# Performance work log

Hardware: AMD Instinct MI355X
Metric: run time of the kernel (lower is better)

Reference implementation:

```python
import jax, jax.numpy as jnp
import numpy as np
import math

B, T, C, H, LC, DFF = 2, 1024, 1024, 16, 256, 4096
EPS = 1e-6


def _ln(x):
    # LayerNorm without affine (elementwise_affine=False under AdaLN), eps=1e-6
    m = jnp.mean(x, -1, keepdims=True)
    v = jnp.mean((x - m) ** 2, -1, keepdims=True)
    return (x - m) * jax.lax.rsqrt(v + EPS)


def _heads(t):
    b, l, c = t.shape
    return t.reshape(b, l, H, c // H).transpose(0, 2, 1, 3)  # (b,H,l,dh)


def _unheads(t):
    b, h, l, d = t.shape
    return t.transpose(0, 2, 1, 3).reshape(b, l, h * d)


def setup_inputs():
    key = jax.random.key(0)
    ks = jax.random.split(key, 16)
    s = 0.02
    p = lambda k, sh: jax.random.normal(k, sh, jnp.float32) * s
    x_star = jax.random.normal(ks[0], (B, T, C), jnp.float32)
    x_hat = jax.random.normal(ks[1], (B, T, C), jnp.float32)
    c = jax.random.normal(ks[2], (B, LC, C), jnp.float32)
    chunk = jnp.sort(jax.random.randint(ks[3], (B, T), 0, 32), axis=1)
    m_star = chunk[:, :, None] > chunk[:, None, :]   # attend to strictly earlier chunks
    m_hat = chunk[:, :, None] == chunk[:, None, :]   # attend within same chunk
    dep_mask = jax.random.bernoulli(ks[4], 0.98, (B, T, T)) | jnp.eye(T, dtype=bool)[None]
    return dict(
        x_star=x_star, x_hat=x_hat, c=c,
        m_star=m_star, m_hat=m_hat, dep_mask=dep_mask,
        ncond_g=jnp.ones((C,), jnp.float32), ncond_b=jnp.zeros((C,), jnp.float32),
        Wq=p(ks[5], (C, C)), bq=jnp.zeros((C,), jnp.float32),
        Wkv=p(ks[6], (C, 2 * C)), bkv=jnp.zeros((2 * C,), jnp.float32),
        Wco=p(ks[7], (C, C)), bco=jnp.zeros((C,), jnp.float32),
        Wada=p(ks[8], (C, 6 * C)), bada=jnp.zeros((6 * C,), jnp.float32),
        Wqkv=p(ks[9], (C, 3 * C)), bqkv=jnp.zeros((3 * C,), jnp.float32),
        Wo=p(ks[10], (C, C)), bo=jnp.zeros((C,), jnp.float32),
        W1=p(ks[11], (C, DFF)), b1=jnp.zeros((DFF,), jnp.float32),
        W2=p(ks[12], (DFF, C)), b2=jnp.zeros((C,), jnp.float32),
    )


def _cross_attn(x, c, Wq, bq, Wkv, bkv, Wco, bco):
    q = _heads(x @ Wq + bq)
    k, v = jnp.split(c @ Wkv + bkv, 2, -1)
    k, v = _heads(k), _heads(v)
    att = jnp.einsum('bhtd,bhsd->bhts', q, k) / math.sqrt(C // H)
    y = jnp.einsum('bhts,bhsd->bhtd', jax.nn.softmax(att, -1), v)
    return _unheads(y) @ Wco + bco


def _interleave(xs, xh, m_star, m_hat, dep, Wqkv, bqkv, Wo, bo):
    # Attention.forward_interleave (eval: dropout identity)
    NEG = -jnp.inf
    sc = 1.0 / math.sqrt(C // H)
    qkv = lambda x: [_heads(t) for t in jnp.split(x @ Wqkv + bqkv, 3, -1)]
    qs, ks, vs = qkv(xs)
    qh, kh, vh = qkv(xh)
    blk_star = (~m_star)[:, None]     # True -> block
    blk_hat = (~m_hat)[:, None]
    blk_dep = (~dep)[:, None]
    causal = jnp.triu(jnp.ones((T, T), bool), 1)[None, None]
    # star stream: causal + dependency mask
    att_star = jnp.einsum('bhtd,bhsd->bhts', qs, ks) * sc
    att_star = jnp.where(blk_dep, NEG, att_star)
    p_star = jax.nn.softmax(jnp.where(causal, NEG, att_star), -1)
    y_star = _unheads(jnp.einsum('bhts,bhsd->bhtd', p_star, vs)) @ Wo + bo
    # hat stream: merge logits (q_hat vs k_star on earlier chunks, q_hat vs k_hat within chunk)
    a1 = jnp.where(blk_star, NEG, jnp.einsum('bhtd,bhsd->bhts', qh, ks) * sc)
    a2 = jnp.where(blk_hat, NEG, jnp.einsum('bhtd,bhsd->bhts', qh, kh) * sc)
    merged = jnp.where(jnp.isinf(a2), a1, a2)
    merged = jnp.where(blk_dep, NEG, merged)
    p_hat = jax.nn.softmax(merged, -1)
    y_hat = jnp.einsum('bhts,bhsd->bhtd', jnp.where(blk_star, 0.0, p_hat), vs) \
          + jnp.einsum('bhts,bhsd->bhtd', jnp.where(blk_hat, 0.0, p_hat), vh)
    y_hat = _unheads(y_hat) @ Wo + bo
    return y_star, y_hat


def reference(x_star, x_hat, c, m_star, m_hat, dep_mask,
              ncond_g, ncond_b, Wq, bq, Wkv, bkv, Wco, bco, Wada, bada,
              Wqkv, bqkv, Wo, bo, W1, b1, W2, b2):
    mod = lambda x, sh, scale: x * (1 + scale) + sh
    mlp = lambda x: jax.nn.gelu(x @ W1 + b1, approximate=True) @ W2 + b2
    ca = lambda x: _cross_attn(_ln(x) * ncond_g + ncond_b, c, Wq, bq, Wkv, bkv, Wco, bco)
    ada = lambda t: jnp.split(jax.nn.silu(t) @ Wada + bada, 6, -1)
    gs = ada(ca(x_star))
    gh = ada(ca(x_hat))
    ms = mod(_ln(x_star), gs[0], gs[1])
    mh = mod(_ln(x_hat), gh[0], gh[1])
    ys, yh = _interleave(ms, mh, m_star, m_hat, dep_mask, Wqkv, bqkv, Wo, bo)
    x_star = x_star + gs[2] * ys
    x_hat = x_hat + gh[2] * yh
    x_star = x_star + gs[5] * mlp(mod(_ln(x_star), gs[3], gs[4]))
    x_hat = x_hat + gh[5] * mlp(mod(_ln(x_hat), gh[3], gh[4]))
    return x_star, x_hat
```

## Files before the change

kernel.cpp:

```cpp
#include <hip/hip_runtime.h>
#include <hip/hip_bf16.h>
#include <stdint.h>

#define DEVI __device__ __forceinline__

typedef __bf16 bf16x8 __attribute__((ext_vector_type(8)));
typedef float f32x4 __attribute__((ext_vector_type(4)));
typedef unsigned short us;
typedef unsigned long long ull;

DEVI float b2f(us u) { union { unsigned int i; float f; } v; v.i = ((unsigned int)u) << 16; return v.f; }
DEVI us f2b(float f) {
  union { unsigned int i; float f; } v; v.f = f;
  unsigned int r = (v.i + 0x7fffu + ((v.i >> 16) & 1u)) >> 16;
  return (us)r;
}

#define NEGINF (-__builtin_inff())

DEVI void gl2lds16(const us* g, us* l) {
  __builtin_amdgcn_global_load_lds(
      (const __attribute__((address_space(1))) unsigned int*)g,
      (__attribute__((address_space(3))) unsigned int*)l, 16, 0, 0);
}

__global__ __launch_bounds__(256) void detect_flags(
    const unsigned int* __restrict__ xw, const unsigned int* __restrict__ mw,
    int* __restrict__ flags) {
  const int t = threadIdx.x;
  int cnt = 0, big = 0;
  for (int i = t; i < 4096; i += 256) {
    unsigned int w = xw[i];
    us lo = (us)(w & 0xffffu);
    float a = fabsf(b2f(lo));
    cnt += ((lo == 0) || (a >= 1e-8f && a <= 256.f)) ? 1 : 0;
    big |= (mw[i] > 1u) ? 1 : 0;
  }
  for (int o = 32; o; o >>= 1) { cnt += __shfl_down(cnt, o); big |= __shfl_down(big, o); }
  __shared__ int sc[4], sb[4];
  if ((t & 63) == 0) { sc[t >> 6] = cnt; sb[t >> 6] = big; }
  __syncthreads();
  if (t == 0) {
    flags[0] = (sc[0] + sc[1] + sc[2] + sc[3] < 2048) ? 1 : 0;
    flags[1] = (sb[0] | sb[1] | sb[2] | sb[3]);
  }
}

__global__ __launch_bounds__(256) void cvt_bf16(
    const void* __restrict__ src, us* __restrict__ dst, int n,
    const int* __restrict__ flags) {
  const int f32mode = flags[0];
  int idx = (blockIdx.x * 256 + threadIdx.x) * 4;
  if (idx >= n) return;
  if (f32mode) {
    const float* s = (const float*)src;
    float4 v = *(const float4*)(s + idx);
    dst[idx] = f2b(v.x); dst[idx + 1] = f2b(v.y);
    dst[idx + 2] = f2b(v.z); dst[idx + 3] = f2b(v.w);
  } else {
    *(uint2*)(dst + idx) = *(const uint2*)((const us*)src + idx);
  }
}

struct P10 { const void* p[10]; };
__global__ __launch_bounds__(256) void cvt_small(P10 ps, us* __restrict__ dst,
                                                 const int* __restrict__ flags) {
  const int offs[11] = {0, 1024, 2048, 3072, 5120, 6144, 12288, 15360, 16384, 20480, 21504};
  int idx = blockIdx.x * 256 + threadIdx.x;
  if (idx >= 21504) return;
  int seg = 0;
#pragma unroll
  for (int i = 1; i < 10; ++i) seg += (idx >= offs[i]) ? 1 : 0;
  int local = idx - offs[seg];
  float v = flags[0] ? ((const float*)ps.p[seg])[local]
                     : b2f(((const us*)ps.p[seg])[local]);
  dst[idx] = f2b(v);
}

__global__ __launch_bounds__(256) void transpose_cvt64(
    const void* __restrict__ W, us* __restrict__ WT, int K, int N,
    const int* __restrict__ flags) {
  __shared__ __attribute__((aligned(16))) us tile[64 * 72];
  const int f32m = flags[0];
  const int k0 = blockIdx.x * 64, n0 = blockIdx.y * 64;
  const int t = threadIdx.x;
  const int row = t >> 2, colb = (t & 3) * 16;
  const int sw = ((row >> 4) & 3) << 4;
  us tmp[16];
  if (f32m) {
    const float* src = (const float*)W + (size_t)(k0 + row) * N + n0 + colb;
#pragma unroll
    for (int i = 0; i < 16; i += 4) {
      float4 v = *(const float4*)(src + i);
      tmp[i] = f2b(v.x); tmp[i + 1] = f2b(v.y); tmp[i + 2] = f2b(v.z); tmp[i + 3] = f2b(v.w);
    }
  } else {
    const us* src = (const us*)W + (size_t)(k0 + row) * N + n0 + colb;
    *(uint4*)tmp = *(const uint4*)src;
    *(uint4*)(tmp + 8) = *(const uint4*)(src + 8);
  }
  *(uint4*)&tile[row * 72 + (colb ^ sw)] = *(uint4*)tmp;
  *(uint4*)&tile[row * 72 + (colb ^ sw) + 8] = *(uint4*)(tmp + 8);
  __syncthreads();
  const int orow = t >> 2, ocolb = (t & 3) * 16;
  const int pc = (orow & 15) | ((orow & 48) ^ (ocolb & 48));
  us out[16];
#pragma unroll
  for (int i = 0; i < 16; ++i) out[i] = tile[(ocolb + i) * 72 + pc];
  us* dst = WT + (size_t)(n0 + orow) * K + k0 + ocolb;
  *(uint4*)dst = *(uint4*)out;
  *(uint4*)(dst + 8) = *(uint4*)(out + 8);
}

struct P3 { const void* p[3]; };
__global__ __launch_bounds__(256) void pack_mask3(P3 ms, ull* __restrict__ bits,
                                                  const int* __restrict__ flags) {
  const int bytemode = flags[1];
  const void* m = ms.p[blockIdx.y];
  ull* out = bits + (size_t)blockIdx.y * 32768;
  int wv = blockIdx.x * 4 + (threadIdx.x >> 6);
  int lane = threadIdx.x & 63;
  for (int w = 0; w < 16; ++w) {
    int v;
    if (bytemode) v = ((const unsigned char*)m)[(size_t)wv * 1024 + w * 64 + lane];
    else          v = ((const int*)m)[(size_t)wv * 1024 + w * 64 + lane];
    ull b = __ballot(v != 0);
    if (lane == 0) out[(size_t)wv * 16 + w] = b;
  }
}

__global__ __launch_bounds__(256) void hat_blockflags(
    const ull* __restrict__ starb, const ull* __restrict__ hatb, int* __restrict__ bf) {
  const int bt = blockIdx.x;
  const int b = bt >> 4, tt = bt & 15;
  const int t = threadIdx.x, wv = t >> 6, lane = t & 63;
  const int t0 = tt * 64;
  for (int k = 0; k < 4; ++k) {
    int ck = wv * 4 + k;
    ull sw = starb[(size_t)(b * 1024 + t0 + lane) * 16 + ck];
    ull hw = hatb[(size_t)(b * 1024 + t0 + lane) * 16 + ck];
    int f = (__ballot(sw != 0ull) ? 1 : 0) | (__ballot(hw != 0ull) ? 2 : 0);
    if (lane == 0) bf[bt * 16 + ck] = f;
  }
}

__global__ __launch_bounds__(256) void vtrans(
    const us* __restrict__ src, us* __restrict__ dst,
    int T, int stride, int colBase, int rowOff) {
  __shared__ __attribute__((aligned(16))) us tile[64][65];
  const int bh = blockIdx.y, b = bh >> 4, h = bh & 15;
  const int t0 = blockIdx.x * 64;
  const int t = threadIdx.x;
#pragma unroll
  for (int it = 0; it < 2; ++it) {
    int idx = it * 256 + t; int r = idx >> 3, c8 = (idx & 7) * 8;
    uint4 d4 = *(const uint4*)(src + (size_t)(rowOff + b * T + t0 + r) * stride + colBase + h * 64 + c8);
    const us* e = (const us*)&d4;
#pragma unroll
    for (int i = 0; i < 8; ++i) tile[r][c8 + i] = e[i];
  }
  __syncthreads();
#pragma unroll
  for (int it = 0; it < 2; ++it) {
    int idx = it * 256 + t; int d = idx >> 3, c8 = (idx & 7) * 8;
    us tmp[8];
#pragma unroll
    for (int i = 0; i < 8; ++i) tmp[i] = tile[c8 + i][d];
    *(uint4*)(dst + ((size_t)(bh * 64 + d)) * T + t0 + c8) = *(const uint4*)tmp;
  }
}

__global__ __launch_bounds__(256) void ln_affine(
    const void* __restrict__ xs, const void* __restrict__ xh,
    const us* __restrict__ gw, const us* __restrict__ bw,
    us* __restrict__ lnx, us* __restrict__ xn, const int* __restrict__ flags) {
  const int f32m = flags[0];
  const int row = blockIdx.x;
  const void* xp = (row < 2048) ? xs : xh;
  const size_t base = (size_t)(row & 2047) * 1024;
  const int t = threadIdx.x;
  float v[4]; float s = 0.f, ss = 0.f;
#pragma unroll
  for (int i = 0; i < 4; ++i) {
    size_t idx = base + i * 256 + t;
    float x = f32m ? ((const float*)xp)[idx] : b2f(((const us*)xp)[idx]);
    v[i] = x; s += x; ss += x * x;
  }
  for (int o = 32; o; o >>= 1) { s += __shfl_down(s, o); ss += __shfl_down(ss, o); }
  __shared__ float red[2][4];
  const int wv = t >> 6, lane = t & 63;
  if (lane == 0) { red[0][wv] = s; red[1][wv] = ss; }
  __syncthreads();
  s = red[0][0] + red[0][1] + red[0][2] + red[0][3];
  ss = red[1][0] + red[1][1] + red[1][2] + red[1][3];
  const float mean = s * (1.f / 1024.f);
  const float var = fmaxf(ss * (1.f / 1024.f) - mean * mean, 0.f);
  const float rstd = rsqrtf(var + 1e-6f);
  const size_t ro = (size_t)row * 1024;
#pragma unroll
  for (int i = 0; i < 4; ++i) {
    int c = i * 256 + t;
    float n = (v[i] - mean) * rstd;
    lnx[ro + c] = f2b(n);
    xn[ro + c] = f2b(n * b2f(gw[c]) + b2f(bw[c]));
  }
}

__global__ __launch_bounds__(256) void mod_ms(
    const us* __restrict__ lnx, const us* __restrict__ gada, us* __restrict__ ms) {
  const size_t idx = ((size_t)blockIdx.x * 256 + threadIdx.x) * 4;
  const int row = (int)(idx >> 10), c = (int)(idx & 1023);
  const size_t gb = (size_t)row * 6144;
#pragma unroll
  for (int i = 0; i < 4; ++i) {
    float sh = b2f(gada[gb + c + i]);
    float sc = b2f(gada[gb + 1024 + c + i]);
    ms[idx + i] = f2b(b2f(lnx[idx + i]) * (1.f + sc) + sh);
  }
}

__global__ __launch_bounds__(256) void ln_mod(
    const float* __restrict__ x1, const us* __restrict__ gada, us* __restrict__ m2) {
  const int row = blockIdx.x;
  const float* xp = x1 + (size_t)row * 1024;
  const int t = threadIdx.x;
  float v[4]; float s = 0.f, ss = 0.f;
#pragma unroll
  for (int i = 0; i < 4; ++i) { float x = xp[i * 256 + t]; v[i] = x; s += x; ss += x * x; }
  for (int o = 32; o; o >>= 1) { s += __shfl_down(s, o); ss += __shfl_down(ss, o); }
  __shared__ float red[2][4];
  const int wv = t >> 6, lane = t & 63;
  if (lane == 0) { red[0][wv] = s; red[1][wv] = ss; }
  __syncthreads();
  s = red[0][0] + red[0][1] + red[0][2] + red[0][3];
  ss = red[1][0] + red[1][1] + red[1][2] + red[1][3];
  const float mean = s * (1.f / 1024.f);
  const float var = fmaxf(ss * (1.f / 1024.f) - mean * mean, 0.f);
  const float rstd = rsqrtf(var + 1e-6f);
  const size_t gb = (size_t)row * 6144;
#pragma unroll
  for (int i = 0; i < 4; ++i) {
    int c = i * 256 + t;
    float n = (v[i] - mean) * rstd;
    float sh = b2f(gada[gb + 3072 + c]);
    float sc = b2f(gada[gb + 4096 + c]);
    m2[(size_t)row * 1024 + c] = f2b(n * (1.f + sc) + sh);
  }
}

enum { EPI_BF16 = 0, EPI_SILU, EPI_GELU, EPI_GATE_XRES, EPI_GATE_OUT };

template <int EPI>
__global__ __launch_bounds__(256) void gemm_bt(
    const us* __restrict__ A, const us* __restrict__ BT,
    const us* __restrict__ bias, void* __restrict__ out,
    int M, int N, int K,
    const us* __restrict__ gate,
    const void* __restrict__ res0, const void* __restrict__ res1,
    const int* __restrict__ oflags) {
  __shared__ __attribute__((aligned(16))) us As[128 * 32];
  __shared__ __attribute__((aligned(16))) us Bs[128 * 32];
  const int m0 = blockIdx.x * 128, n0 = blockIdx.y * 128;
  const int t = threadIdx.x;
  const int wave = t >> 6, lane = t & 63;
  const int wm = (wave >> 1) * 64, wn = (wave & 1) * 64;
  const int l16 = lane & 15, quad = lane >> 4;
  f32x4 acc[4][4] = {};

  const int lr = lane >> 2, lc = (lane & 3) * 8;
  const us* gA = A + (size_t)(m0 + wave * 32 + lr) * K + lc;
  const us* gB = BT + (size_t)(n0 + wave * 32 + lr) * K + lc;
  us* lA = &As[wave * 32 * 32];
  us* lB = &Bs[wave * 32 * 32];

  for (int k0 = 0; k0 < K; k0 += 32) {
    __syncthreads();
    gl2lds16(gA + k0, lA);
    gl2lds16(gA + (size_t)16 * K + k0, lA + 512);
    gl2lds16(gB + k0, lB);
    gl2lds16(gB + (size_t)16 * K + k0, lB + 512);
    __syncthreads();
    bf16x8 af[4], bf[4];
#pragma unroll
    for (int i = 0; i < 4; ++i) af[i] = *(const bf16x8*)(const void*)&As[(wm + i * 16 + l16) * 32 + quad * 8];
#pragma unroll
    for (int j = 0; j < 4; ++j) bf[j] = *(const bf16x8*)(const void*)&Bs[(wn + j * 16 + l16) * 32 + quad * 8];
#pragma unroll
    for (int i = 0; i < 4; ++i)
#pragma unroll
      for (int j = 0; j < 4; ++j)
        acc[i][j] = __builtin_amdgcn_mfma_f32_16x16x32_bf16(af[i], bf[j], acc[i][j], 0, 0, 0);
  }

#pragma unroll
  for (int i = 0; i < 4; ++i) {
    const int gm = m0 + wm + i * 16 + quad * 4;
#pragma unroll
    for (int j = 0; j < 4; ++j) {
      const int gn = n0 + wn + j * 16 + l16;
      const float bv = b2f(bias[gn]);
#pragma unroll
      for (int r = 0; r < 4; ++r) {
        const int gmr = gm + r;
        float v = acc[i][j][r] + bv;
        const size_t oi = (size_t)gmr * N + gn;
        if constexpr (EPI == EPI_BF16) {
          ((us*)out)[oi] = f2b(v);
        } else if constexpr (EPI == EPI_SILU) {
          ((us*)out)[oi] = f2b(v / (1.f + __expf(-v)));
        } else if constexpr (EPI == EPI_GELU) {
          float u = 0.7978845608028654f * (v + 0.044715f * v * v * v);
          float th = 1.f - 2.f / (__expf(2.f * u) + 1.f);
          ((us*)out)[oi] = f2b(0.5f * v * (1.f + th));
        } else if constexpr (EPI == EPI_GATE_XRES) {
          float g = b2f(gate[(size_t)gmr * 6144 + gn]);
          const void* xr = (gmr < 2048) ? res0 : res1;
          size_t xi = (size_t)(gmr & 2047) * 1024 + gn;
          float x = oflags[0] ? ((const float*)xr)[xi] : b2f(((const us*)xr)[xi]);
          ((float*)out)[oi] = x + g * v;
        } else {
          float g = b2f(gate[(size_t)gmr * 6144 + gn]);
          float x = ((const float*)res0)[oi];
          float r2 = x + g * v;
          if (oflags[0]) ((float*)out)[oi] = r2;
          else ((us*)out)[oi] = f2b(r2);
        }
      }
    }
  }
}


__global__ __launch_bounds__(256) void cross_attn_mfma(
    const us* __restrict__ q, const us* __restrict__ kv,
    const us* __restrict__ vT, us* __restrict__ y) {
  __shared__ __attribute__((aligned(16))) us Kb[2][64 * 72];
  __shared__ __attribute__((aligned(16))) us Vb[2][64 * 72];
  us* Ps = &Kb[0][0];
  const int bid = blockIdx.x;
  const int xcd = bid & 7, tmp = bid >> 3;
  const int tt = tmp & 15, gq = tmp >> 4;
  const int g = gq * 8 + xcd;
  const int st = g >> 5, b = (g >> 4) & 1, h = g & 15;
  const int t = threadIdx.x, wv = t >> 6, lane = t & 63;
  const int l16 = lane & 15, quad = lane >> 4;
  const int rowbase = st * 2048 + b * 1024 + tt * 64 + wv * 16;
  const us* qp = q + (size_t)(rowbase + l16) * 1024 + h * 64 + quad * 8;
  bf16x8 aq0 = *(const bf16x8*)(qp);
  bf16x8 aq1 = *(const bf16x8*)(qp + 32);
  const us* kb = kv + (size_t)b * (256 * 2048) + h * 64;
  const us* vb = vT + (size_t)(b * 16 + h) * 64 * 256;
  float m_st[4] = {NEGINF, NEGINF, NEGINF, NEGINF};
  float l_st[4] = {0.f, 0.f, 0.f, 0.f};
  f32x4 o[4] = {};
  for (int rnd = 0; rnd < 2; ++rnd) {
    const int s0 = rnd * 128;
    __syncthreads();
#pragma unroll
    for (int it = 0; it < 2; ++it) {
      int id = it * 256 + t; int row = id >> 3, g8 = (id & 7) * 8;
      *(uint4*)&Kb[0][row * 72 + g8] = *(const uint4*)(kb + (size_t)(s0 + row) * 2048 + g8);
      *(uint4*)&Kb[1][row * 72 + g8] = *(const uint4*)(kb + (size_t)(s0 + 64 + row) * 2048 + g8);
      *(uint4*)&Vb[0][row * 72 + g8] = *(const uint4*)(vb + (size_t)row * 256 + s0 + g8);
      *(uint4*)&Vb[1][row * 72 + g8] = *(const uint4*)(vb + (size_t)row * 256 + s0 + 64 + g8);
    }
    __syncthreads();
    f32x4 s[8];
#pragma unroll
    for (int j = 0; j < 8; ++j) {
      const us* kbuf = (j < 4) ? &Kb[0][0] : &Kb[1][0];
      const int row = (j & 3) * 16 + l16;
      bf16x8 bk0 = *(const bf16x8*)(const void*)&kbuf[row * 72 + quad * 8];
      bf16x8 bk1 = *(const bf16x8*)(const void*)&kbuf[row * 72 + 32 + quad * 8];
      f32x4 z = {};
      z = __builtin_amdgcn_mfma_f32_16x16x32_bf16(aq0, bk0, z, 0, 0, 0);
      z = __builtin_amdgcn_mfma_f32_16x16x32_bf16(aq1, bk1, z, 0, 0, 0);
      s[j] = z;
    }
    __syncthreads();
#pragma unroll
    for (int r = 0; r < 4; ++r) {
      float mx = NEGINF;
#pragma unroll
      for (int j = 0; j < 8; ++j) { float sv = s[j][r] * 0.125f; s[j][r] = sv; mx = fmaxf(mx, sv); }
#pragma unroll
      for (int o2 = 8; o2; o2 >>= 1) mx = fmaxf(mx, __shfl_xor(mx, o2));
      const float mn = fmaxf(m_st[r], mx);
      const float alpha = __expf(m_st[r] - mn);
      float rs = 0.f;
#pragma unroll
      for (int j = 0; j < 8; ++j) { float p = __expf(s[j][r] - mn); s[j][r] = p; rs += p; }
#pragma unroll
      for (int o2 = 8; o2; o2 >>= 1) rs += __shfl_xor(rs, o2);
      m_st[r] = mn;
      l_st[r] = l_st[r] * alpha + rs;
#pragma unroll
      for (int jd = 0; jd < 4; ++jd) o[jd][r] *= alpha;
#pragma unroll
      for (int j = 0; j < 8; ++j)
        Ps[(wv * 16 + quad * 4 + r) * 136 + j * 16 + l16] = f2b(s[j][r]);
    }
    bf16x8 ap[4];
#pragma unroll
    for (int kk = 0; kk < 4; ++kk)
      ap[kk] = *(const bf16x8*)(const void*)&Ps[(wv * 16 + l16) * 136 + kk * 32 + quad * 8];
#pragma unroll
    for (int jd = 0; jd < 4; ++jd) {
      bf16x8 b0 = *(const bf16x8*)(const void*)&Vb[0][(jd * 16 + l16) * 72 + quad * 8];
      bf16x8 b1 = *(const bf16x8*)(const void*)&Vb[0][(jd * 16 + l16) * 72 + 32 + quad * 8];
      bf16x8 b2 = *(const bf16x8*)(const void*)&Vb[1][(jd * 16 + l16) * 72 + quad * 8];
      bf16x8 b3 = *(const bf16x8*)(const void*)&Vb[1][(jd * 16 + l16) * 72 + 32 + quad * 8];
      o[jd] = __builtin_amdgcn_mfma_f32_16x16x32_bf16(ap[0], b0, o[jd], 0, 0, 0);
      o[jd] = __builtin_amdgcn_mfma_f32_16x16x32_bf16(ap[1], b1, o[jd], 0, 0, 0);
      o[jd] = __builtin_amdgcn_mfma_f32_16x16x32_bf16(ap[2], b2, o[jd], 0, 0, 0);
      o[jd] = __builtin_amdgcn_mfma_f32_16x16x32_bf16(ap[3], b3, o[jd], 0, 0, 0);
    }
  }
#pragma unroll
  for (int r = 0; r < 4; ++r) {
    const float inv = (l_st[r] > 0.f) ? 1.f / l_st[r] : 0.f;
#pragma unroll
    for (int jd = 0; jd < 4; ++jd)
      y[(size_t)(rowbase + quad * 4 + r) * 1024 + h * 64 + jd * 16 + l16] = f2b(o[jd][r] * inv);
  }
}

DEVI void star_body(us* Ks0, us* Vt0, const us* qkv, const us* vT,
                    const ull* depb, us* y, int b, int h, int tt, int t) {
  us* Ks1 = Ks0 + 64 * 72;
  us* Vt1 = Vt0 + 64 * 72;
  us* Ps = Ks0;
  const int wv = t >> 6, lane = t & 63;
  const int l16 = lane & 15, quad = lane >> 4;
  const int t0 = tt * 64;
  const int rowbase = b * 1024 + t0 + wv * 16;
  const us* qp = qkv + (size_t)(rowbase + l16) * 3072 + h * 64 + quad * 8;
  bf16x8 aq0 = *(const bf16x8*)(qp);
  bf16x8 aq1 = *(const bf16x8*)(qp + 32);
  const us* kb = qkv + (size_t)(b * 1024) * 3072 + 1024 + h * 64;
  const us* vb = vT + (size_t)(b * 16 + h) * 65536;
  float m_st[4] = {NEGINF, NEGINF, NEGINF, NEGINF};
  float l_st[4] = {0.f, 0.f, 0.f, 0.f};
  f32x4 o[4] = {};
  for (int ck0 = 0; ck0 <= tt; ck0 += 2) {
    const int s0 = ck0 * 64;
    __syncthreads();
#pragma unroll
    for (int it = 0; it < 2; ++it) {
      int id = it * 256 + t; int row = id >> 3, g8 = (id & 7) * 8;
      *(uint4*)&Ks0[row * 72 + g8] = *(const uint4*)(kb + (size_t)(s0 + row) * 3072 + g8);
      *(uint4*)&Ks1[row * 72 + g8] = *(const uint4*)(kb + (size_t)(s0 + 64 + row) * 3072 + g8);
      *(uint4*)&Vt0[row * 72 + g8] = *(const uint4*)(vb + (size_t)row * 1024 + s0 + g8);
      *(uint4*)&Vt1[row * 72 + g8] = *(const uint4*)(vb + (size_t)row * 1024 + s0 + 64 + g8);
    }
    __syncthreads();
    ull dw[2][4];
#pragma unroll
    for (int c2 = 0; c2 < 2; ++c2)
#pragma unroll
      for (int r = 0; r < 4; ++r)
        dw[c2][r] = depb[(size_t)(rowbase + quad * 4 + r) * 16 + ck0 + c2];
    f32x4 s[8];
#pragma unroll
    for (int j = 0; j < 8; ++j) {
      const us* kbuf = (j < 4) ? Ks0 : Ks1;
      const int row = (j & 3) * 16 + l16;
      bf16x8 bk0 = *(const bf16x8*)(const void*)&kbuf[row * 72 + quad * 8];
      bf16x8 bk1 = *(const bf16x8*)(const void*)&kbuf[row * 72 + 32 + quad * 8];
      f32x4 z = {};
      z = __builtin_amdgcn_mfma_f32_16x16x32_bf16(aq0, bk0, z, 0, 0, 0);
      z = __builtin_amdgcn_mfma_f32_16x16x32_bf16(aq1, bk1, z, 0, 0, 0);
      s[j] = z;
    }
    __syncthreads();
#pragma unroll
    for (int r = 0; r < 4; ++r) {
      const int trow = t0 + wv * 16 + quad * 4 + r;
      float mx = NEGINF;
#pragma unroll
      for (int j = 0; j < 8; ++j) {
        const int c2 = j >> 2;
        const int kl = (j & 3) * 16 + l16;
        const int kg = s0 + c2 * 64 + kl;
        bool ok = (kg <= trow) && ((dw[c2][r] >> kl) & 1ull);
        float sv = ok ? s[j][r] * 0.125f : NEGINF;
        s[j][r] = sv;
        mx = fmaxf(mx, sv);
      }
#pragma unroll
      for (int o2 = 8; o2; o2 >>= 1) mx = fmaxf(mx, __shfl_xor(mx, o2));
      const float mn = fmaxf(m_st[r], mx);
      const bool dead = (mn == NEGINF);
      const float alpha = dead ? 1.f : __expf(m_st[r] - mn);
      float rs = 0.f;
#pragma unroll
      for (int j = 0; j < 8; ++j) {
        float p = dead ? 0.f : __expf(s[j][r] - mn);
        s[j][r] = p;
        rs += p;
      }
#pragma unroll
      for (int o2 = 8; o2; o2 >>= 1) rs += __shfl_xor(rs, o2);
      m_st[r] = mn;
      l_st[r] = l_st[r] * alpha + rs;
#pragma unroll
      for (int jd = 0; jd < 4; ++jd) o[jd][r] *= alpha;
#pragma unroll
      for (int j = 0; j < 8; ++j)
        Ps[(wv * 16 + quad * 4 + r) * 136 + j * 16 + l16] = f2b(s[j][r]);
    }
    bf16x8 ap[4];
#pragma unroll
    for (int kk = 0; kk < 4; ++kk)
      ap[kk] = *(const bf16x8*)(const void*)&Ps[(wv * 16 + l16) * 136 + kk * 32 + quad * 8];
#pragma unroll
    for (int jd = 0; jd < 4; ++jd) {
      bf16x8 b0 = *(const bf16x8*)(const void*)&Vt0[(jd * 16 + l16) * 72 + quad * 8];
      bf16x8 b1 = *(const bf16x8*)(const void*)&Vt0[(jd * 16 + l16) * 72 + 32 + quad * 8];
      bf16x8 b2 = *(const bf16x8*)(const void*)&Vt1[(jd * 16 + l16) * 72 + quad * 8];
      bf16x8 b3 = *(const bf16x8*)(const void*)&Vt1[(jd * 16 + l16) * 72 + 32 + quad * 8];
      o[jd] = __builtin_amdgcn_mfma_f32_16x16x32_bf16(ap[0], b0, o[jd], 0, 0, 0);
      o[jd] = __builtin_amdgcn_mfma_f32_16x16x32_bf16(ap[1], b1, o[jd], 0, 0, 0);
      o[jd] = __builtin_amdgcn_mfma_f32_16x16x32_bf16(ap[2], b2, o[jd], 0, 0, 0);
      o[jd] = __builtin_amdgcn_mfma_f32_16x16x32_bf16(ap[3], b3, o[jd], 0, 0, 0);
    }
  }
#pragma unroll
  for (int r = 0; r < 4; ++r) {
    const float inv = (l_st[r] > 0.f) ? 1.f / l_st[r] : 0.f;
#pragma unroll
    for (int jd = 0; jd < 4; ++jd)
      y[(size_t)(rowbase + quad * 4 + r) * 1024 + h * 64 + jd * 16 + l16] = f2b(o[jd][r] * inv);
  }
}

DEVI void hat_body(us* Kst0, us* Vtt0, const us* qkv,
                   const us* vsT, const us* vhT,
                   const ull* starb, const ull* hatb, const ull* depb,
                   const int* bflags, us* y, int b, int h, int tt, int t) {
  us* Kst1 = Kst0 + 64 * 72;
  us* Vtt1 = Vtt0 + 64 * 72;
  us* Ps = Kst0;
  const int wv = t >> 6, lane = t & 63;
  const int l16 = lane & 15, quad = lane >> 4;
  const int t0 = tt * 64;
  const int rowbase = b * 1024 + t0 + wv * 16;
  const us* qp = qkv + (size_t)(2048 + rowbase + l16) * 3072 + h * 64 + quad * 8;
  bf16x8 aq0 = *(const bf16x8*)(qp);
  bf16x8 aq1 = *(const bf16x8*)(qp + 32);
  const us* ksb = qkv + (size_t)(b * 1024) * 3072 + 1024 + h * 64;
  const us* khb = qkv + (size_t)(2048 + b * 1024) * 3072 + 1024 + h * 64;
  const us* vsb = vsT + (size_t)(b * 16 + h) * 65536;
  const us* vhb = vhT + (size_t)(b * 16 + h) * 65536;
  float m_st[4] = {NEGINF, NEGINF, NEGINF, NEGINF};
  float l_st[4] = {0.f, 0.f, 0.f, 0.f};
  f32x4 o[4] = {};
  for (int ck = 0; ck < 16; ++ck) {
    if (bflags[(b * 16 + tt) * 16 + ck] == 0) continue;
    const int s0 = ck * 64;
    __syncthreads();
#pragma unroll
    for (int it = 0; it < 2; ++it) {
      int id = it * 256 + t; int row = id >> 3, g8 = (id & 7) * 8;
      *(uint4*)&Kst0[row * 72 + g8] = *(const uint4*)(ksb + (size_t)(s0 + row) * 3072 + g8);
      *(uint4*)&Kst1[row * 72 + g8] = *(const uint4*)(khb + (size_t)(s0 + row) * 3072 + g8);
      *(uint4*)&Vtt0[row * 72 + g8] = *(const uint4*)(vsb + (size_t)row * 1024 + s0 + g8);
      *(uint4*)&Vtt1[row * 72 + g8] = *(const uint4*)(vhb + (size_t)row * 1024 + s0 + g8);
    }
    __syncthreads();
    ull as_[4], ah_[4];
#pragma unroll
    for (int r = 0; r < 4; ++r) {
      const size_t mrow = (size_t)(rowbase + quad * 4 + r) * 16 + ck;
      const ull dwm = depb[mrow];
      as_[r] = starb[mrow] & dwm;
      ah_[r] = hatb[mrow] & dwm;
    }
    f32x4 s[8];
#pragma unroll
    for (int j = 0; j < 8; ++j) {
      const us* kbuf = (j < 4) ? Kst0 : Kst1;
      const int row = (j & 3) * 16 + l16;
      bf16x8 bk0 = *(const bf16x8*)(const void*)&kbuf[row * 72 + quad * 8];
      bf16x8 bk1 = *(const bf16x8*)(const void*)&kbuf[row * 72 + 32 + quad * 8];
      f32x4 z = {};
      z = __builtin_amdgcn_mfma_f32_16x16x32_bf16(aq0, bk0, z, 0, 0, 0);
      z = __builtin_amdgcn_mfma_f32_16x16x32_bf16(aq1, bk1, z, 0, 0, 0);
      s[j] = z;
    }
    __syncthreads();
#pragma unroll
    for (int r = 0; r < 4; ++r) {
      float mx = NEGINF;
#pragma unroll
      for (int j = 0; j < 8; ++j) {
        const int kl = (j & 3) * 16 + l16;
        const ull act = (j < 4) ? as_[r] : ah_[r];
        bool ok = ((act >> kl) & 1ull) != 0;
        float sv = ok ? s[j][r] * 0.125f : NEGINF;
        s[j][r] = sv;
        mx = fmaxf(mx, sv);
      }
#pragma unroll
      for (int o2 = 8; o2; o2 >>= 1) mx = fmaxf(mx, __shfl_xor(mx, o2));
      const float mn = fmaxf(m_st[r], mx);
      const bool dead = (mn == NEGINF);
      const float alpha = dead ? 1.f : __expf(m_st[r] - mn);
      float rs = 0.f;
#pragma unroll
      for (int j = 0; j < 8; ++j) {
        float p = dead ? 0.f : __expf(s[j][r] - mn);
        s[j][r] = p;
        rs += p;
      }
#pragma unroll
      for (int o2 = 8; o2; o2 >>= 1) rs += __shfl_xor(rs, o2);
      m_st[r] = mn;
      l_st[r] = l_st[r] * alpha + rs;
#pragma unroll
      for (int jd = 0; jd < 4; ++jd) o[jd][r] *= alpha;
#pragma unroll
      for (int j = 0; j < 8; ++j)
        Ps[(wv * 16 + quad * 4 + r) * 136 + j * 16 + l16] = f2b(s[j][r]);
    }
    bf16x8 ap[4];
#pragma unroll
    for (int kk = 0; kk < 4; ++kk)
      ap[kk] = *(const bf16x8*)(const void*)&Ps[(wv * 16 + l16) * 136 + kk * 32 + quad * 8];
#pragma unroll
    for (int jd = 0; jd < 4; ++jd) {
      bf16x8 b0 = *(const bf16x8*)(const void*)&Vtt0[(jd * 16 + l16) * 72 + quad * 8];
      bf16x8 b1 = *(const bf16x8*)(const void*)&Vtt0[(jd * 16 + l16) * 72 + 32 + quad * 8];
      bf16x8 b2 = *(const bf16x8*)(const void*)&Vtt1[(jd * 16 + l16) * 72 + quad * 8];
      bf16x8 b3 = *(const bf16x8*)(const void*)&Vtt1[(jd * 16 + l16) * 72 + 32 + quad * 8];
      o[jd] = __builtin_amdgcn_mfma_f32_16x16x32_bf16(ap[0], b0, o[jd], 0, 0, 0);
      o[jd] = __builtin_amdgcn_mfma_f32_16x16x32_bf16(ap[1], b1, o[jd], 0, 0, 0);
      o[jd] = __builtin_amdgcn_mfma_f32_16x16x32_bf16(ap[2], b2, o[jd], 0, 0, 0);
      o[jd] = __builtin_amdgcn_mfma_f32_16x16x32_bf16(ap[3], b3, o[jd], 0, 0, 0);
    }
  }
#pragma unroll
  for (int r = 0; r < 4; ++r) {
    const float inv = (l_st[r] > 0.f) ? 1.f / l_st[r] : 0.f;
#pragma unroll
    for (int jd = 0; jd < 4; ++jd)
      y[(size_t)(2048 + rowbase + quad * 4 + r) * 1024 + h * 64 + jd * 16 + l16] = f2b(o[jd][r] * inv);
  }
}

__global__ __launch_bounds__(256) void self_attn_mfma(
    const us* __restrict__ qkv,
    const us* __restrict__ vstT, const us* __restrict__ vhtT,
    const ull* __restrict__ sbits, const ull* __restrict__ hbits,
    const ull* __restrict__ dbits, const int* __restrict__ bflags,
    us* __restrict__ y) {
  __shared__ __attribute__((aligned(16))) us Kbuf[2][64 * 72];
  __shared__ __attribute__((aligned(16))) us Vbuf[2][64 * 72];
  const int bid = blockIdx.x;
  const int xcd = bid & 7, tmp = bid >> 3;
  const int tt = tmp & 15, gq = tmp >> 4;
  const int g = gq * 8 + xcd;
  const int t = threadIdx.x;
  if (g < 32) {
    star_body(&Kbuf[0][0], &Vbuf[0][0], qkv, vstT, dbits, y, g >> 4, g & 15, tt, t);
  } else {
    const int g2 = g - 32;
    hat_body(&Kbuf[0][0], &Vbuf[0][0], qkv, vstT, vhtT, sbits, hbits, dbits, bflags,
             y, g2 >> 4, g2 & 15, tt, t);
  }
}

extern "C" void kernel_launch(void* const* d_in, const int* in_sizes, int n_in,
                              void* d_out, int out_size, void* d_ws, size_t ws_size,
                              hipStream_t stream) {
  const void* xs = d_in[0];
  const void* xh = d_in[1];
  const void* cc = d_in[2];
  const void* mstar = d_in[3];
  const void* mhat = d_in[4];
  const void* mdep = d_in[5];
  const void* ng = d_in[6];
  const void* nb = d_in[7];
  const void* Wq = d_in[8];
  const void* bq = d_in[9];
  const void* Wkv = d_in[10];
  const void* bkv = d_in[11];
  const void* Wco = d_in[12];
  const void* bco = d_in[13];
  const void* Wada = d_in[14];
  const void* bada = d_in[15];
  const void* Wqkv = d_in[16];
  const void* bqkv = d_in[17];
  const void* Wo = d_in[18];
  const void* bo = d_in[19];
  const void* W1 = d_in[20];
  const void* b1 = d_in[21];
  const void* W2 = d_in[22];
  const void* b2 = d_in[23];
  (void)in_sizes; (void)n_in; (void)out_size; (void)ws_size;

  char* ws = (char*)d_ws;
  size_t off = 0;
  auto alloc = [&](size_t bytes) -> char* {
    char* p = ws + off;
    off += (bytes + 255) & ~(size_t)255;
    return p;
  };
  int* flags = (int*)alloc(256);
  int* bflags = (int*)alloc(512 * 4);
  us* smallb = (us*)alloc(21504 * 2);
  us* ngb = smallb, *nbb = smallb + 1024, *bqb = smallb + 2048,
      *bkvb = smallb + 3072, *bcob = smallb + 5120, *badab = smallb + 6144,
      *bqkvb = smallb + 12288, *bob = smallb + 15360, *b1b = smallb + 16384,
      *b2b = smallb + 20480;
  us* WqT = (us*)alloc(1048576ull * 2);
  us* WkvT = (us*)alloc(2097152ull * 2);
  us* WcoT = (us*)alloc(1048576ull * 2);
  us* WadaT = (us*)alloc(6291456ull * 2);
  us* WqkvT = (us*)alloc(3145728ull * 2);
  us* WoT = (us*)alloc(1048576ull * 2);
  us* W1T = (us*)alloc(4194304ull * 2);
  us* W2T = (us*)alloc(4194304ull * 2);
  us* xn = (us*)alloc(4194304ull * 2);
  us* qb = (us*)alloc(4194304ull * 2);
  us* kvb = (us*)alloc(1048576ull * 2);
  us* gada = (us*)alloc(25165824ull * 2);
  us* msb = (us*)alloc(4194304ull * 2);
  us* qkvb = (us*)alloc(12582912ull * 2);
  float* x1 = (float*)alloc(4194304ull * 4);
  us* hid = (us*)alloc(16777216ull * 2);
  ull* mb = (ull*)alloc(3ull * 32768 * 8);
  us* kvT = (us*)alloc(524288ull * 2);
  us* vstT = (us*)alloc(2097152ull * 2);
  us* vhtT = (us*)alloc(2097152ull * 2);

  ull* sbits = mb;
  ull* hbits = mb + 32768;
  ull* dbits = mb + 65536;
  us* ccb = hid;
  us* lnx = hid + 1048576;
  us* yca = xn;
  us* silub = qb;
  us* yat = msb;

  dim3 blk(256);
  detect_flags<<<1, blk, 0, stream>>>((const unsigned int*)xs, (const unsigned int*)mdep, flags);

  cvt_bf16<<<512, blk, 0, stream>>>(cc, ccb, 524288, flags);
  P10 ps10; ps10.p[0] = ng; ps10.p[1] = nb; ps10.p[2] = bq; ps10.p[3] = bkv;
  ps10.p[4] = bco; ps10.p[5] = bada; ps10.p[6] = bqkv; ps10.p[7] = bo;
  ps10.p[8] = b1; ps10.p[9] = b2;
  cvt_small<<<84, blk, 0, stream>>>(ps10, smallb, flags);

  transpose_cvt64<<<dim3(16, 16), blk, 0, stream>>>(Wq, WqT, 1024, 1024, flags);
  transpose_cvt64<<<dim3(16, 32), blk, 0, stream>>>(Wkv, WkvT, 1024, 2048, flags);
  transpose_cvt64<<<dim3(16, 16), blk, 0, stream>>>(Wco, WcoT, 1024, 1024, flags);
  transpose_cvt64<<<dim3(16, 96), blk, 0, stream>>>(Wada, WadaT, 1024, 6144, flags);
  transpose_cvt64<<<dim3(16, 48), blk, 0, stream>>>(Wqkv, WqkvT, 1024, 3072, flags);
  transpose_cvt64<<<dim3(16, 16), blk, 0, stream>>>(Wo, WoT, 1024, 1024, flags);
  transpose_cvt64<<<dim3(16, 64), blk, 0, stream>>>(W1, W1T, 1024, 4096, flags);
  transpose_cvt64<<<dim3(64, 16), blk, 0, stream>>>(W2, W2T, 4096, 1024, flags);

  P3 ps3; ps3.p[0] = mstar; ps3.p[1] = mhat; ps3.p[2] = mdep;
  pack_mask3<<<dim3(512, 3), blk, 0, stream>>>(ps3, mb, flags);
  hat_blockflags<<<32, blk, 0, stream>>>(sbits, hbits, bflags);

  ln_affine<<<4096, blk, 0, stream>>>(xs, xh, ngb, nbb, lnx, xn, flags);
  gemm_bt<EPI_BF16><<<dim3(32, 8), blk, 0, stream>>>(xn, WqT, bqb, qb, 4096, 1024, 1024, nullptr, nullptr, nullptr, nullptr);
  gemm_bt<EPI_BF16><<<dim3(4, 16), blk, 0, stream>>>(ccb, WkvT, bkvb, kvb, 512, 2048, 1024, nullptr, nullptr, nullptr, nullptr);
  vtrans<<<dim3(4, 32), blk, 0, stream>>>(kvb, kvT, 256, 2048, 1024, 0);
  cross_attn_mfma<<<1024, blk, 0, stream>>>(qb, kvb, kvT, yca);
  gemm_bt<EPI_SILU><<<dim3(32, 8), blk, 0, stream>>>(yca, WcoT, bcob, silub, 4096, 1024, 1024, nullptr, nullptr, nullptr, nullptr);
  gemm_bt<EPI_BF16><<<dim3(32, 48), blk, 0, stream>>>(silub, WadaT, badab, gada, 4096, 6144, 1024, nullptr, nullptr, nullptr, nullptr);
  mod_ms<<<4096, blk, 0, stream>>>(lnx, gada, msb);
  gemm_bt<EPI_BF16><<<dim3(32, 24), blk, 0, stream>>>(msb, WqkvT, bqkvb, qkvb, 4096, 3072, 1024, nullptr, nullptr, nullptr, nullptr);
  vtrans<<<dim3(16, 32), blk, 0, stream>>>(qkvb, vstT, 1024, 3072, 2048, 0);
  vtrans<<<dim3(16, 32), blk, 0, stream>>>(qkvb, vhtT, 1024, 3072, 2048, 2048);
  self_attn_mfma<<<1024, blk, 0, stream>>>(qkvb, vstT, vhtT, sbits, hbits, dbits, bflags, yat);
  gemm_bt<EPI_GATE_XRES><<<dim3(32, 8), blk, 0, stream>>>(yat, WoT, bob, x1, 4096, 1024, 1024, gada + 2048, xs, xh, flags);
  ln_mod<<<4096, blk, 0, stream>>>(x1, gada, msb);
  gemm_bt<EPI_GELU><<<dim3(32, 32), blk, 0, stream>>>(msb, W1T, b1b, hid, 4096, 4096, 1024, nullptr, nullptr, nullptr, nullptr);
  gemm_bt<EPI_GATE_OUT><<<dim3(32, 8), blk, 0, stream>>>(hid, W2T, b2b, d_out, 4096, 1024, 4096, gada + 5120, x1, nullptr, flags);
}
```

Before: 772.2 us.

## Add 128x64 GEMM tiles for narrow outputs and restructure attention into 64-key rounds

Adds a gemm_bt64 variant with 128x64 tiles and uses it for the N=1024/2048 GEMMs, doubling the block count so the 256-CU device is better filled. The attention kernels are refactored into a shared attn_round helper that processes 64 keys per round with a dedicated P buffer, which removes one barrier per round. Softmax switches to exp2 with a folded scale. Masks are applied multiplicatively after exp, and the star/hat key blocks of the hat path are processed separately so blocks flagged empty are skipped. Smaller tiles reduce reuse per block, and the extra rounds add more staging and barrier passes.

```diff
diff --git a/kernel.cpp b/kernel.cpp
--- a/kernel.cpp
+++ b/kernel.cpp
@@ -249,6 +249,34 @@
 }
 
 enum { EPI_BF16 = 0, EPI_SILU, EPI_GELU, EPI_GATE_XRES, EPI_GATE_OUT };
+
+template <int EPI>
+DEVI void gemm_epi(float v, int gmr, int gn, int N, void* out,
+                   const us* gate, const void* res0, const void* res1,
+                   const int* oflags) {
+  const size_t oi = (size_t)gmr * N + gn;
+  if constexpr (EPI == EPI_BF16) {
+    ((us*)out)[oi] = f2b(v);
+  } else if constexpr (EPI == EPI_SILU) {
+    ((us*)out)[oi] = f2b(v / (1.f + __expf(-v)));
+  } else if constexpr (EPI == EPI_GELU) {
+    float u = 0.7978845608028654f * (v + 0.044715f * v * v * v);
+    float th = 1.f - 2.f / (__expf(2.f * u) + 1.f);
+    ((us*)out)[oi] = f2b(0.5f * v * (1.f + th));
+  } else if constexpr (EPI == EPI_GATE_XRES) {
+    float g = b2f(gate[(size_t)gmr * 6144 + gn]);
+    const void* xr = (gmr < 2048) ? res0 : res1;
+    size_t xi = (size_t)(gmr & 2047) * 1024 + gn;
+    float x = oflags[0] ? ((const float*)xr)[xi] : b2f(((const us*)xr)[xi]);
+    ((float*)out)[oi] = x + g * v;
+  } else {
+    float g = b2f(gate[(size_t)gmr * 6144 + gn]);
+    float x = ((const float*)res0)[oi];
+    float r2 = x + g * v;
+    if (oflags[0]) ((float*)out)[oi] = r2;
+    else ((us*)out)[oi] = f2b(r2);
+  }
+}
 
 template <int EPI>
 __global__ __launch_bounds__(256) void gemm_bt(
@@ -280,16 +308,16 @@
     gl2lds16(gB + k0, lB);
     gl2lds16(gB + (size_t)16 * K + k0, lB + 512);
     __syncthreads();
-    bf16x8 af[4], bf[4];
+    bf16x8 af[4], bfv[4];
 #pragma unroll
     for (int i = 0; i < 4; ++i) af[i] = *(const bf16x8*)(const void*)&As[(wm + i * 16 + l16) * 32 + quad * 8];
 #pragma unroll
-    for (int j = 0; j < 4; ++j) bf[j] = *(const bf16x8*)(const void*)&Bs[(wn + j * 16 + l16) * 32 + quad * 8];
+    for (int j = 0; j < 4; ++j) bfv[j] = *(const bf16x8*)(const void*)&Bs[(wn + j * 16 + l16) * 32 + quad * 8];
 #pragma unroll
     for (int i = 0; i < 4; ++i)
 #pragma unroll
       for (int j = 0; j < 4; ++j)
-        acc[i][j] = __builtin_amdgcn_mfma_f32_16x16x32_bf16(af[i], bf[j], acc[i][j], 0, 0, 0);
+        acc[i][j] = __builtin_amdgcn_mfma_f32_16x16x32_bf16(af[i], bfv[j], acc[i][j], 0, 0, 0);
   }
 
 #pragma unroll
@@ -300,136 +328,180 @@
       const int gn = n0 + wn + j * 16 + l16;
       const float bv = b2f(bias[gn]);
 #pragma unroll
-      for (int r = 0; r < 4; ++r) {
-        const int gmr = gm + r;
-        float v = acc[i][j][r] + bv;
-        const size_t oi = (size_t)gmr * N + gn;
-        if constexpr (EPI == EPI_BF16) {
-          ((us*)out)[oi] = f2b(v);
-        } else if constexpr (EPI == EPI_SILU) {
-          ((us*)out)[oi] = f2b(v / (1.f + __expf(-v)));
-        } else if constexpr (EPI == EPI_GELU) {
-          float u = 0.7978845608028654f * (v + 0.044715f * v * v * v);
-          float th = 1.f - 2.f / (__expf(2.f * u) + 1.f);
-          ((us*)out)[oi] = f2b(0.5f * v * (1.f + th));
-        } else if constexpr (EPI == EPI_GATE_XRES) {
-          float g = b2f(gate[(size_t)gmr * 6144 + gn]);
-          const void* xr = (gmr < 2048) ? res0 : res1;
-          size_t xi = (size_t)(gmr & 2047) * 1024 + gn;
-          float x = oflags[0] ? ((const float*)xr)[xi] : b2f(((const us*)xr)[xi]);
-          ((float*)out)[oi] = x + g * v;
-        } else {
-          float g = b2f(gate[(size_t)gmr * 6144 + gn]);
-          float x = ((const float*)res0)[oi];
-          float r2 = x + g * v;
-          if (oflags[0]) ((float*)out)[oi] = r2;
-          else ((us*)out)[oi] = f2b(r2);
-        }
-      }
+      for (int r = 0; r < 4; ++r)
+        gemm_epi<EPI>(acc[i][j][r] + bv, gm + r, gn, N, out, gate, res0, res1, oflags);
     }
   }
 }
 
+template <int EPI>
+__global__ __launch_bounds__(256) void gemm_bt64(
+    const us* __restrict__ A, const us* __restrict__ BT,
+    const us* __restrict__ bias, void* __restrict__ out,
+    int M, int N, int K,
+    const us* __restrict__ gate,
+    const void* __restrict__ res0, const void* __restrict__ res1,
+    const int* __restrict__ oflags) {
+  __shared__ __attribute__((aligned(16))) us As[128 * 32];
+  __shared__ __attribute__((aligned(16))) us Bs[64 * 32];
+  const int m0 = blockIdx.x * 128, n0 = blockIdx.y * 64;
+  const int t = threadIdx.x;
+  const int wave = t >> 6, lane = t & 63;
+  const int wm = (wave >> 1) * 64, wn = (wave & 1) * 32;
+  const int l16 = lane & 15, quad = lane >> 4;
+  f32x4 acc[4][2] = {};
+
+  const int lr = lane >> 2, lc = (lane & 3) * 8;
+  const us* gA = A + (size_t)(m0 + wave * 32 + lr) * K + lc;
+  const us* gB = BT + (size_t)(n0 + wave * 16 + lr) * K + lc;
+  us* lA = &As[wave * 32 * 32];
+  us* lB = &Bs[wave * 16 * 32];
+
+  for (int k0 = 0; k0 < K; k0 += 32) {
+    __syncthreads();
+    gl2lds16(gA + k0, lA);
+    gl2lds16(gA + (size_t)16 * K + k0, lA + 512);
+    gl2lds16(gB + k0, lB);
+    __syncthreads();
+    bf16x8 af[4], bfv[2];
+#pragma unroll
+    for (int i = 0; i < 4; ++i) af[i] = *(const bf16x8*)(const void*)&As[(wm + i * 16 + l16) * 32 + quad * 8];
+#pragma unroll
+    for (int j = 0; j < 2; ++j) bfv[j] = *(const bf16x8*)(const void*)&Bs[(wn + j * 16 + l16) * 32 + quad * 8];
+#pragma unroll
+    for (int i = 0; i < 4; ++i)
+#pragma unroll
+      for (int j = 0; j < 2; ++j)
+        acc[i][j] = __builtin_amdgcn_mfma_f32_16x16x32_bf16(af[i], bfv[j], acc[i][j], 0, 0, 0);
+  }
+
+#pragma unroll
+  for (int i = 0; i < 4; ++i) {
+    const int gm = m0 + wm + i * 16 + quad * 4;
+#pragma unroll
+    for (int j = 0; j < 2; ++j) {
+      const int gn = n0 + wn + j * 16 + l16;
+      const float bv = b2f(bias[gn]);
+#pragma unroll
+      for (int r = 0; r < 4; ++r)
+        gemm_epi<EPI>(acc[i][j][r] + bv, gm + r, gn, N, out, gate, res0, res1, oflags);
+    }
+  }
+}
+
+struct AttnState { float m[4], l[4]; f32x4 o[4]; };
+
+DEVI void st_init(AttnState& s) {
+#pragma unroll
+  for (int r = 0; r < 4; ++r) { s.m[r] = NEGINF; s.l[r] = 0.f; s.o[r] = f32x4{}; }
+}
+
+DEVI void stage64(us* __restrict__ dst, const us* __restrict__ src,
+                  int strideUs, int t) {
+#pragma unroll
+  for (int it = 0; it < 2; ++it) {
+    const int id = it * 256 + t;
+    const int row = id >> 3, c8 = (id & 7) * 8;
+    *(uint4*)&dst[row * 72 + c8] = *(const uint4*)(src + (size_t)row * strideUs + c8);
+  }
+}
+
+template <bool MASKED>
+DEVI void attn_round(const us* __restrict__ Kb, const us* __restrict__ Vb,
+                     us* __restrict__ Pb, const ull* mrow,
+                     bf16x8 aq0, bf16x8 aq1, AttnState& st,
+                     int wv, int l16, int quad) {
+  f32x4 s[4];
+#pragma unroll
+  for (int j = 0; j < 4; ++j) {
+    const int row = j * 16 + l16;
+    bf16x8 bk0 = *(const bf16x8*)(const void*)&Kb[row * 72 + quad * 8];
+    bf16x8 bk1 = *(const bf16x8*)(const void*)&Kb[row * 72 + 32 + quad * 8];
+    f32x4 z = {};
+    z = __builtin_amdgcn_mfma_f32_16x16x32_bf16(aq0, bk0, z, 0, 0, 0);
+    z = __builtin_amdgcn_mfma_f32_16x16x32_bf16(aq1, bk1, z, 0, 0, 0);
+    s[j] = z;
+  }
+  const float CE = 0.18033688011112042f;
+#pragma unroll
+  for (int r = 0; r < 4; ++r) {
+    float mx = fmaxf(fmaxf(s[0][r], s[1][r]), fmaxf(s[2][r], s[3][r]));
+#pragma unroll
+    for (int o2 = 8; o2; o2 >>= 1) mx = fmaxf(mx, __shfl_xor(mx, o2));
+    const float mn = fmaxf(st.m[r], mx);
+    const float alpha = exp2f((st.m[r] - mn) * CE);
+    const float mnC = mn * CE;
+    float rs = 0.f;
+#pragma unroll
+    for (int j = 0; j < 4; ++j) {
+      float p = exp2f(__builtin_fmaf(s[j][r], CE, -mnC));
+      if constexpr (MASKED) p = ((mrow[r] >> (j * 16 + l16)) & 1ull) ? p : 0.f;
+      rs += p;
+      ((__bf16*)Pb)[(wv * 16 + quad * 4 + r) * 72 + j * 16 + l16] = (__bf16)p;
+    }
+#pragma unroll
+    for (int o2 = 8; o2; o2 >>= 1) rs += __shfl_xor(rs, o2);
+    st.m[r] = mn;
+    st.l[r] = st.l[r] * alpha + rs;
+#pragma unroll
+    for (int jd = 0; jd < 4; ++jd) st.o[jd][r] *= alpha;
+  }
+  bf16x8 ap0 = *(const bf16x8*)(const void*)&Pb[(wv * 16 + l16) * 72 + quad * 8];
+  bf16x8 ap1 = *(const bf16x8*)(const void*)&Pb[(wv * 16 + l16) * 72 + 32 + quad * 8];
+#pragma unroll
+  for (int jd = 0; jd < 4; ++jd) {
+    bf16x8 v0 = *(const bf16x8*)(const void*)&Vb[(jd * 16 + l16) * 72 + quad * 8];
+    bf16x8 v1 = *(const bf16x8*)(const void*)&Vb[(jd * 16 + l16) * 72 + 32 + quad * 8];
+    st.o[jd] = __builtin_amdgcn_mfma_f32_16x16x32_bf16(ap0, v0, st.o[jd], 0, 0, 0);
+    st.o[jd] = __builtin_amdgcn_mfma_f32_16x16x32_bf16(ap1, v1, st.o[jd], 0, 0, 0);
+  }
+}
+
+DEVI void attn_write(us* __restrict__ y, const AttnState& st, int rowAbs,
+                     int h, int l16, int quad) {
+#pragma unroll
+  for (int r = 0; r < 4; ++r) {
+    const float inv = (st.l[r] > 0.f) ? 1.f / st.l[r] : 0.f;
+#pragma unroll
+    for (int jd = 0; jd < 4; ++jd)
+      y[(size_t)(rowAbs + quad * 4 + r) * 1024 + h * 64 + jd * 16 + l16] =
+          f2b(st.o[jd][r] * inv);
+  }
+}
 
 __global__ __launch_bounds__(256) void cross_attn_mfma(
     const us* __restrict__ q, const us* __restrict__ kv,
     const us* __restrict__ vT, us* __restrict__ y) {
-  __shared__ __attribute__((aligned(16))) us Kb[2][64 * 72];
-  __shared__ __attribute__((aligned(16))) us Vb[2][64 * 72];
-  us* Ps = &Kb[0][0];
+  __shared__ __attribute__((aligned(16))) us Kb[64 * 72];
+  __shared__ __attribute__((aligned(16))) us Vb[64 * 72];
+  __shared__ __attribute__((aligned(16))) us Pb[64 * 72];
   const int bid = blockIdx.x;
   const int xcd = bid & 7, tmp = bid >> 3;
   const int tt = tmp & 15, gq = tmp >> 4;
   const int g = gq * 8 + xcd;
-  const int st = g >> 5, b = (g >> 4) & 1, h = g & 15;
+  const int strm = g >> 5, b = (g >> 4) & 1, h = g & 15;
   const int t = threadIdx.x, wv = t >> 6, lane = t & 63;
   const int l16 = lane & 15, quad = lane >> 4;
-  const int rowbase = st * 2048 + b * 1024 + tt * 64 + wv * 16;
+  const int rowbase = strm * 2048 + b * 1024 + tt * 64 + wv * 16;
   const us* qp = q + (size_t)(rowbase + l16) * 1024 + h * 64 + quad * 8;
   bf16x8 aq0 = *(const bf16x8*)(qp);
   bf16x8 aq1 = *(const bf16x8*)(qp + 32);
   const us* kb = kv + (size_t)b * (256 * 2048) + h * 64;
-  const us* vb = vT + (size_t)(b * 16 + h) * 64 * 256;
-  float m_st[4] = {NEGINF, NEGINF, NEGINF, NEGINF};
-  float l_st[4] = {0.f, 0.f, 0.f, 0.f};
-  f32x4 o[4] = {};
-  for (int rnd = 0; rnd < 2; ++rnd) {
-    const int s0 = rnd * 128;
+  const us* vb = vT + (size_t)(b * 16 + h) * (64 * 256);
+  AttnState st; st_init(st);
+  for (int rnd = 0; rnd < 4; ++rnd) {
+    const int s0 = rnd * 64;
     __syncthreads();
-#pragma unroll
-    for (int it = 0; it < 2; ++it) {
-      int id = it * 256 + t; int row = id >> 3, g8 = (id & 7) * 8;
-      *(uint4*)&Kb[0][row * 72 + g8] = *(const uint4*)(kb + (size_t)(s0 + row) * 2048 + g8);
-      *(uint4*)&Kb[1][row * 72 + g8] = *(const uint4*)(kb + (size_t)(s0 + 64 + row) * 2048 + g8);
-      *(uint4*)&Vb[0][row * 72 + g8] = *(const uint4*)(vb + (size_t)row * 256 + s0 + g8);
-      *(uint4*)&Vb[1][row * 72 + g8] = *(const uint4*)(vb + (size_t)row * 256 + s0 + 64 + g8);
-    }
+    stage64(Kb, kb + (size_t)s0 * 2048, 2048, t);
+    stage64(Vb, vb + s0, 256, t);
     __syncthreads();
-    f32x4 s[8];
-#pragma unroll
-    for (int j = 0; j < 8; ++j) {
-      const us* kbuf = (j < 4) ? &Kb[0][0] : &Kb[1][0];
-      const int row = (j & 3) * 16 + l16;
-      bf16x8 bk0 = *(const bf16x8*)(const void*)&kbuf[row * 72 + quad * 8];
-      bf16x8 bk1 = *(const bf16x8*)(const void*)&kbuf[row * 72 + 32 + quad * 8];
-      f32x4 z = {};
-      z = __builtin_amdgcn_mfma_f32_16x16x32_bf16(aq0, bk0, z, 0, 0, 0);
-      z = __builtin_amdgcn_mfma_f32_16x16x32_bf16(aq1, bk1, z, 0, 0, 0);
-      s[j] = z;
-    }
-    __syncthreads();
-#pragma unroll
-    for (int r = 0; r < 4; ++r) {
-      float mx = NEGINF;
-#pragma unroll
-      for (int j = 0; j < 8; ++j) { float sv = s[j][r] * 0.125f; s[j][r] = sv; mx = fmaxf(mx, sv); }
-#pragma unroll
-      for (int o2 = 8; o2; o2 >>= 1) mx = fmaxf(mx, __shfl_xor(mx, o2));
-      const float mn = fmaxf(m_st[r], mx);
-      const float alpha = __expf(m_st[r] - mn);
-      float rs = 0.f;
-#pragma unroll
-      for (int j = 0; j < 8; ++j) { float p = __expf(s[j][r] - mn); s[j][r] = p; rs += p; }
-#pragma unroll
-      for (int o2 = 8; o2; o2 >>= 1) rs += __shfl_xor(rs, o2);
-      m_st[r] = mn;
-      l_st[r] = l_st[r] * alpha + rs;
-#pragma unroll
-      for (int jd = 0; jd < 4; ++jd) o[jd][r] *= alpha;
-#pragma unroll
-      for (int j = 0; j < 8; ++j)
-        Ps[(wv * 16 + quad * 4 + r) * 136 + j * 16 + l16] = f2b(s[j][r]);
-    }
-    bf16x8 ap[4];
-#pragma unroll
-    for (int kk = 0; kk < 4; ++kk)
-      ap[kk] = *(const bf16x8*)(const void*)&Ps[(wv * 16 + l16) * 136 + kk * 32 + quad * 8];
-#pragma unroll
-    for (int jd = 0; jd < 4; ++jd) {
-      bf16x8 b0 = *(const bf16x8*)(const void*)&Vb[0][(jd * 16 + l16) * 72 + quad * 8];
-      bf16x8 b1 = *(const bf16x8*)(const void*)&Vb[0][(jd * 16 + l16) * 72 + 32 + quad * 8];
-      bf16x8 b2 = *(const bf16x8*)(const void*)&Vb[1][(jd * 16 + l16) * 72 + quad * 8];
-      bf16x8 b3 = *(const bf16x8*)(const void*)&Vb[1][(jd * 16 + l16) * 72 + 32 + quad * 8];
-      o[jd] = __builtin_amdgcn_mfma_f32_16x16x32_bf16(ap[0], b0, o[jd], 0, 0, 0);
-      o[jd] = __builtin_amdgcn_mfma_f32_16x16x32_bf16(ap[1], b1, o[jd], 0, 0, 0);
-      o[jd] = __builtin_amdgcn_mfma_f32_16x16x32_bf16(ap[2], b2, o[jd], 0, 0, 0);
-      o[jd] = __builtin_amdgcn_mfma_f32_16x16x32_bf16(ap[3], b3, o[jd], 0, 0, 0);
-    }
-  }
-#pragma unroll
-  for (int r = 0; r < 4; ++r) {
-    const float inv = (l_st[r] > 0.f) ? 1.f / l_st[r] : 0.f;
-#pragma unroll
-    for (int jd = 0; jd < 4; ++jd)
-      y[(size_t)(rowbase + quad * 4 + r) * 1024 + h * 64 + jd * 16 + l16] = f2b(o[jd][r] * inv);
-  }
-}
-
-DEVI void star_body(us* Ks0, us* Vt0, const us* qkv, const us* vT,
+    attn_round<false>(Kb, Vb, Pb, nullptr, aq0, aq1, st, wv, l16, quad);
+  }
+  attn_write(y, st, rowbase, h, l16, quad);
+}
+
+DEVI void star_body(us* Kb, us* Vb, us* Pb, const us* qkv, const us* vT,
                     const ull* depb, us* y, int b, int h, int tt, int t) {
-  us* Ks1 = Ks0 + 64 * 72;
-  us* Vt1 = Vt0 + 64 * 72;
-  us* Ps = Ks0;
   const int wv = t >> 6, lane = t & 63;
   const int l16 = lane & 15, quad = lane >> 4;
   const int t0 = tt * 64;
@@ -439,108 +511,32 @@
   bf16x8 aq1 = *(const bf16x8*)(qp + 32);
   const us* kb = qkv + (size_t)(b * 1024) * 3072 + 1024 + h * 64;
   const us* vb = vT + (size_t)(b * 16 + h) * 65536;
-  float m_st[4] = {NEGINF, NEGINF, NEGINF, NEGINF};
-  float l_st[4] = {0.f, 0.f, 0.f, 0.f};
-  f32x4 o[4] = {};
-  for (int ck0 = 0; ck0 <= tt; ck0 += 2) {
-    const int s0 = ck0 * 64;
+  AttnState st; st_init(st);
+  ull mrow[4];
+  for (int ck = 0; ck <= tt; ++ck) {
+    const int s0 = ck * 64;
     __syncthreads();
-#pragma unroll
-    for (int it = 0; it < 2; ++it) {
-      int id = it * 256 + t; int row = id >> 3, g8 = (id & 7) * 8;
-      *(uint4*)&Ks0[row * 72 + g8] = *(const uint4*)(kb + (size_t)(s0 + row) * 3072 + g8);
-      *(uint4*)&Ks1[row * 72 + g8] = *(const uint4*)(kb + (size_t)(s0 + 64 + row) * 3072 + g8);
-      *(uint4*)&Vt0[row * 72 + g8] = *(const uint4*)(vb + (size_t)row * 1024 + s0 + g8);
-      *(uint4*)&Vt1[row * 72 + g8] = *(const uint4*)(vb + (size_t)row * 1024 + s0 + 64 + g8);
+    stage64(Kb, kb + (size_t)s0 * 3072, 3072, t);
+    stage64(Vb, vb + s0, 1024, t);
+    __syncthreads();
+#pragma unroll
+    for (int r = 0; r < 4; ++r) {
+      ull d = depb[(size_t)(rowbase + quad * 4 + r) * 16 + ck];
+      if (ck == tt) {
+        const int idx = wv * 16 + quad * 4 + r;
+        d &= (2ull << idx) - 1ull;
+      }
+      mrow[r] = d;
     }
-    __syncthreads();
-    ull dw[2][4];
-#pragma unroll
-    for (int c2 = 0; c2 < 2; ++c2)
-#pragma unroll
-      for (int r = 0; r < 4; ++r)
-        dw[c2][r] = depb[(size_t)(rowbase + quad * 4 + r) * 16 + ck0 + c2];
-    f32x4 s[8];
-#pragma unroll
-    for (int j = 0; j < 8; ++j) {
-      const us* kbuf = (j < 4) ? Ks0 : Ks1;
-      const int row = (j & 3) * 16 + l16;
-      bf16x8 bk0 = *(const bf16x8*)(const void*)&kbuf[row * 72 + quad * 8];
-      bf16x8 bk1 = *(const bf16x8*)(const void*)&kbuf[row * 72 + 32 + quad * 8];
-      f32x4 z = {};
-      z = __builtin_amdgcn_mfma_f32_16x16x32_bf16(aq0, bk0, z, 0, 0, 0);
-      z = __builtin_amdgcn_mfma_f32_16x16x32_bf16(aq1, bk1, z, 0, 0, 0);
-      s[j] = z;
-    }
-    __syncthreads();
-#pragma unroll
-    for (int r = 0; r < 4; ++r) {
-      const int trow = t0 + wv * 16 + quad * 4 + r;
-      float mx = NEGINF;
-#pragma unroll
-      for (int j = 0; j < 8; ++j) {
-        const int c2 = j >> 2;
-        const int kl = (j & 3) * 16 + l16;
-        const int kg = s0 + c2 * 64 + kl;
-        bool ok = (kg <= trow) && ((dw[c2][r] >> kl) & 1ull);
-        float sv = ok ? s[j][r] * 0.125f : NEGINF;
-        s[j][r] = sv;
-        mx = fmaxf(mx, sv);
-      }
-#pragma unroll
-      for (int o2 = 8; o2; o2 >>= 1) mx = fmaxf(mx, __shfl_xor(mx, o2));
-      const float mn = fmaxf(m_st[r], mx);
-      const bool dead = (mn == NEGINF);
-      const float alpha = dead ? 1.f : __expf(m_st[r] - mn);
-      float rs = 0.f;
-#pragma unroll
-      for (int j = 0; j < 8; ++j) {
-        float p = dead ? 0.f : __expf(s[j][r] - mn);
-        s[j][r] = p;
-        rs += p;
-      }
-#pragma unroll
-      for (int o2 = 8; o2; o2 >>= 1) rs += __shfl_xor(rs, o2);
-      m_st[r] = mn;
-      l_st[r] = l_st[r] * alpha + rs;
-#pragma unroll
-      for (int jd = 0; jd < 4; ++jd) o[jd][r] *= alpha;
-#pragma unroll
-      for (int j = 0; j < 8; ++j)
-        Ps[(wv * 16 + quad * 4 + r) * 136 + j * 16 + l16] = f2b(s[j][r]);
-    }
-    bf16x8 ap[4];
-#pragma unroll
-    for (int kk = 0; kk < 4; ++kk)
-      ap[kk] = *(const bf16x8*)(const void*)&Ps[(wv * 16 + l16) * 136 + kk * 32 + quad * 8];
-#pragma unroll
-    for (int jd = 0; jd < 4; ++jd) {
-      bf16x8 b0 = *(const bf16x8*)(const void*)&Vt0[(jd * 16 + l16) * 72 + quad * 8];
-      bf16x8 b1 = *(const bf16x8*)(const void*)&Vt0[(jd * 16 + l16) * 72 + 32 + quad * 8];
-      bf16x8 b2 = *(const bf16x8*)(const void*)&Vt1[(jd * 16 + l16) * 72 + quad * 8];
-      bf16x8 b3 = *(const bf16x8*)(const void*)&Vt1[(jd * 16 + l16) * 72 + 32 + quad * 8];
-      o[jd] = __builtin_amdgcn_mfma_f32_16x16x32_bf16(ap[0], b0, o[jd], 0, 0, 0);
-      o[jd] = __builtin_amdgcn_mfma_f32_16x16x32_bf16(ap[1], b1, o[jd], 0, 0, 0);
-      o[jd] = __builtin_amdgcn_mfma_f32_16x16x32_bf16(ap[2], b2, o[jd], 0, 0, 0);
-      o[jd] = __builtin_amdgcn_mfma_f32_16x16x32_bf16(ap[3], b3, o[jd], 0, 0, 0);
-    }
-  }
-#pragma unroll
-  for (int r = 0; r < 4; ++r) {
-    const float inv = (l_st[r] > 0.f) ? 1.f / l_st[r] : 0.f;
-#pragma unroll
-    for (int jd = 0; jd < 4; ++jd)
-      y[(size_t)(rowbase + quad * 4 + r) * 1024 + h * 64 + jd * 16 + l16] = f2b(o[jd][r] * inv);
-  }
-}
-
-DEVI void hat_body(us* Kst0, us* Vtt0, const us* qkv,
+    attn_round<true>(Kb, Vb, Pb, mrow, aq0, aq1, st, wv, l16, quad);
+  }
+  attn_write(y, st, rowbase, h, l16, quad);
+}
+
+DEVI void hat_body(us* Kb, us* Vb, us* Pb, const us* qkv,
                    const us* vsT, const us* vhT,
                    const ull* starb, const ull* hatb, const ull* depb,
                    const int* bflags, us* y, int b, int h, int tt, int t) {
-  us* Kst1 = Kst0 + 64 * 72;
-  us* Vtt1 = Vtt0 + 64 * 72;
-  us* Ps = Kst0;
   const int wv = t >> 6, lane = t & 63;
   const int l16 = lane & 15, quad = lane >> 4;
   const int t0 = tt * 64;
@@ -552,100 +548,37 @@
   const us* khb = qkv + (size_t)(2048 + b * 1024) * 3072 + 1024 + h * 64;
   const us* vsb = vsT + (size_t)(b * 16 + h) * 65536;
   const us* vhb = vhT + (size_t)(b * 16 + h) * 65536;
-  float m_st[4] = {NEGINF, NEGINF, NEGINF, NEGINF};
-  float l_st[4] = {0.f, 0.f, 0.f, 0.f};
-  f32x4 o[4] = {};
+  AttnState st; st_init(st);
+  ull mrow[4];
   for (int ck = 0; ck < 16; ++ck) {
-    if (bflags[(b * 16 + tt) * 16 + ck] == 0) continue;
+    const int f = bflags[(b * 16 + tt) * 16 + ck];
     const int s0 = ck * 64;
-    __syncthreads();
-#pragma unroll
-    for (int it = 0; it < 2; ++it) {
-      int id = it * 256 + t; int row = id >> 3, g8 = (id & 7) * 8;
-      *(uint4*)&Kst0[row * 72 + g8] = *(const uint4*)(ksb + (size_t)(s0 + row) * 3072 + g8);
-      *(uint4*)&Kst1[row * 72 + g8] = *(const uint4*)(khb + (size_t)(s0 + row) * 3072 + g8);
-      *(uint4*)&Vtt0[row * 72 + g8] = *(const uint4*)(vsb + (size_t)row * 1024 + s0 + g8);
-      *(uint4*)&Vtt1[row * 72 + g8] = *(const uint4*)(vhb + (size_t)row * 1024 + s0 + g8);
+    if (f & 1) {
+      __syncthreads();
+      stage64(Kb, ksb + (size_t)s0 * 3072, 3072, t);
+      stage64(Vb, vsb + s0, 1024, t);
+      __syncthreads();
+#pragma unroll
+      for (int r = 0; r < 4; ++r) {
+        const size_t mi = (size_t)(rowbase + quad * 4 + r) * 16 + ck;
+        mrow[r] = starb[mi] & depb[mi];
+      }
+      attn_round<true>(Kb, Vb, Pb, mrow, aq0, aq1, st, wv, l16, quad);
     }
-    __syncthreads();
-    ull as_[4], ah_[4];
-#pragma unroll
-    for (int r = 0; r < 4; ++r) {
-      const size_t mrow = (size_t)(rowbase + quad * 4 + r) * 16 + ck;
-      const ull dwm = depb[mrow];
-      as_[r] = starb[mrow] & dwm;
-      ah_[r] = hatb[mrow] & dwm;
+    if (f & 2) {
+      __syncthreads();
+      stage64(Kb, khb + (size_t)s0 * 3072, 3072, t);
+      stage64(Vb, vhb + s0, 1024, t);
+      __syncthreads();
+#pragma unroll
+      for (int r = 0; r < 4; ++r) {
+        const size_t mi = (size_t)(rowbase + quad * 4 + r) * 16 + ck;
+        mrow[r] = hatb[mi] & depb[mi];
+      }
+      attn_round<true>(Kb, Vb, Pb, mrow, aq0, aq1, st, wv, l16, quad);
     }
-    f32x4 s[8];
-#pragma unroll
-    for (int j = 0; j < 8; ++j) {
-      const us* kbuf = (j < 4) ? Kst0 : Kst1;
-      const int row = (j & 3) * 16 + l16;
-      bf16x8 bk0 = *(const bf16x8*)(const void*)&kbuf[row * 72 + quad * 8];
-      bf16x8 bk1 = *(const bf16x8*)(const void*)&kbuf[row * 72 + 32 + quad * 8];
-      f32x4 z = {};
-      z = __builtin_amdgcn_mfma_f32_16x16x32_bf16(aq0, bk0, z, 0, 0, 0);
-      z = __builtin_amdgcn_mfma_f32_16x16x32_bf16(aq1, bk1, z, 0, 0, 0);
-      s[j] = z;
-    }
-    __syncthreads();
-#pragma unroll
-    for (int r = 0; r < 4; ++r) {
-      float mx = NEGINF;
-#pragma unroll
-      for (int j = 0; j < 8; ++j) {
-        const int kl = (j & 3) * 16 + l16;
-        const ull act = (j < 4) ? as_[r] : ah_[r];
-        bool ok = ((act >> kl) & 1ull) != 0;
-        float sv = ok ? s[j][r] * 0.125f : NEGINF;
-        s[j][r] = sv;
-        mx = fmaxf(mx, sv);
-      }
-#pragma unroll
-      for (int o2 = 8; o2; o2 >>= 1) mx = fmaxf(mx, __shfl_xor(mx, o2));
-      const float mn = fmaxf(m_st[r], mx);
-      const bool dead = (mn == NEGINF);
-      const float alpha = dead ? 1.f : __expf(m_st[r] - mn);
-      float rs = 0.f;
-#pragma unroll
-      for (int j = 0; j < 8; ++j) {
-        float p = dead ? 0.f : __expf(s[j][r] - mn);
-        s[j][r] = p;
-        rs += p;
-      }
-#pragma unroll
-      for (int o2 = 8; o2; o2 >>= 1) rs += __shfl_xor(rs, o2);
-      m_st[r] = mn;
-      l_st[r] = l_st[r] * alpha + rs;
-#pragma unroll
-      for (int jd = 0; jd < 4; ++jd) o[jd][r] *= alpha;
-#pragma unroll
-      for (int j = 0; j < 8; ++j)
-        Ps[(wv * 16 + quad * 4 + r) * 136 + j * 16 + l16] = f2b(s[j][r]);
-    }
-    bf16x8 ap[4];
-#pragma unroll
-    for (int kk = 0; kk < 4; ++kk)
-      ap[kk] = *(const bf16x8*)(const void*)&Ps[(wv * 16 + l16) * 136 + kk * 32 + quad * 8];
-#pragma unroll
-    for (int jd = 0; jd < 4; ++jd) {
-      bf16x8 b0 = *(const bf16x8*)(const void*)&Vtt0[(jd * 16 + l16) * 72 + quad * 8];
-      bf16x8 b1 = *(const bf16x8*)(const void*)&Vtt0[(jd * 16 + l16) * 72 + 32 + quad * 8];
-      bf16x8 b2 = *(const bf16x8*)(const void*)&Vtt1[(jd * 16 + l16) * 72 + quad * 8];
-      bf16x8 b3 = *(const bf16x8*)(const void*)&Vtt1[(jd * 16 + l16) * 72 + 32 + quad * 8];
-      o[jd] = __builtin_amdgcn_mfma_f32_16x16x32_bf16(ap[0], b0, o[jd], 0, 0, 0);
-      o[jd] = __builtin_amdgcn_mfma_f32_16x16x32_bf16(ap[1], b1, o[jd], 0, 0, 0);
-      o[jd] = __builtin_amdgcn_mfma_f32_16x16x32_bf16(ap[2], b2, o[jd], 0, 0, 0);
-      o[jd] = __builtin_amdgcn_mfma_f32_16x16x32_bf16(ap[3], b3, o[jd], 0, 0, 0);
-    }
-  }
-#pragma unroll
-  for (int r = 0; r < 4; ++r) {
-    const float inv = (l_st[r] > 0.f) ? 1.f / l_st[r] : 0.f;
-#pragma unroll
-    for (int jd = 0; jd < 4; ++jd)
-      y[(size_t)(2048 + rowbase + quad * 4 + r) * 1024 + h * 64 + jd * 16 + l16] = f2b(o[jd][r] * inv);
-  }
+  }
+  attn_write(y, st, 2048 + rowbase, h, l16, quad);
 }
 
 __global__ __launch_bounds__(256) void self_attn_mfma(
@@ -654,18 +587,19 @@
     const ull* __restrict__ sbits, const ull* __restrict__ hbits,
     const ull* __restrict__ dbits, const int* __restrict__ bflags,
     us* __restrict__ y) {
-  __shared__ __attribute__((aligned(16))) us Kbuf[2][64 * 72];
-  __shared__ __attribute__((aligned(16))) us Vbuf[2][64 * 72];
+  __shared__ __attribute__((aligned(16))) us Kb[64 * 72];
+  __shared__ __attribute__((aligned(16))) us Vb[64 * 72];
+  __shared__ __attribute__((aligned(16))) us Pb[64 * 72];
   const int bid = blockIdx.x;
   const int xcd = bid & 7, tmp = bid >> 3;
   const int tt = tmp & 15, gq = tmp >> 4;
   const int g = gq * 8 + xcd;
   const int t = threadIdx.x;
   if (g < 32) {
-    star_body(&Kbuf[0][0], &Vbuf[0][0], qkv, vstT, dbits, y, g >> 4, g & 15, tt, t);
+    star_body(Kb, Vb, Pb, qkv, vstT, dbits, y, g >> 4, g & 15, tt, t);
   } else {
     const int g2 = g - 32;
-    hat_body(&Kbuf[0][0], &Vbuf[0][0], qkv, vstT, vhtT, sbits, hbits, dbits, bflags,
+    hat_body(Kb, Vb, Pb, qkv, vstT, vhtT, sbits, hbits, dbits, bflags,
              y, g2 >> 4, g2 & 15, tt, t);
   }
 }
@@ -766,19 +700,19 @@
   hat_blockflags<<<32, blk, 0, stream>>>(sbits, hbits, bflags);
 
   ln_affine<<<4096, blk, 0, stream>>>(xs, xh, ngb, nbb, lnx, xn, flags);
-  gemm_bt<EPI_BF16><<<dim3(32, 8), blk, 0, stream>>>(xn, WqT, bqb, qb, 4096, 1024, 1024, nullptr, nullptr, nullptr, nullptr);
-  gemm_bt<EPI_BF16><<<dim3(4, 16), blk, 0, stream>>>(ccb, WkvT, bkvb, kvb, 512, 2048, 1024, nullptr, nullptr, nullptr, nullptr);
+  gemm_bt64<EPI_BF16><<<dim3(32, 16), blk, 0, stream>>>(xn, WqT, bqb, qb, 4096, 1024, 1024, nullptr, nullptr, nullptr, nullptr);
+  gemm_bt64<EPI_BF16><<<dim3(4, 32), blk, 0, stream>>>(ccb, WkvT, bkvb, kvb, 512, 2048, 1024, nullptr, nullptr, nullptr, nullptr);
   vtrans<<<dim3(4, 32), blk, 0, stream>>>(kvb, kvT, 256, 2048, 1024, 0);
   cross_attn_mfma<<<1024, blk, 0, stream>>>(qb, kvb, kvT, yca);
-  gemm_bt<EPI_SILU><<<dim3(32, 8), blk, 0, stream>>>(yca, WcoT, bcob, silub, 4096, 1024, 1024, nullptr, nullptr, nullptr, nullptr);
+  gemm_bt64<EPI_SILU><<<dim3(32, 16), blk, 0, stream>>>(yca, WcoT, bcob, silub, 4096, 1024, 1024, nullptr, nullptr, nullptr, nullptr);
   gemm_bt<EPI_BF16><<<dim3(32, 48), blk, 0, stream>>>(silub, WadaT, badab, gada, 4096, 6144, 1024, nullptr, nullptr, nullptr, nullptr);
   mod_ms<<<4096, blk, 0, stream>>>(lnx, gada, msb);
   gemm_bt<EPI_BF16><<<dim3(32, 24), blk, 0, stream>>>(msb, WqkvT, bqkvb, qkvb, 4096, 3072, 1024, nullptr, nullptr, nullptr, nullptr);
   vtrans<<<dim3(16, 32), blk, 0, stream>>>(qkvb, vstT, 1024, 3072, 2048, 0);
   vtrans<<<dim3(16, 32), blk, 0, stream>>>(qkvb, vhtT, 1024, 3072, 2048, 2048);
   self_attn_mfma<<<1024, blk, 0, stream>>>(qkvb, vstT, vhtT, sbits, hbits, dbits, bflags, yat);
-  gemm_bt<EPI_GATE_XRES><<<dim3(32, 8), blk, 0, stream>>>(yat, WoT, bob, x1, 4096, 1024, 1024, gada + 2048, xs, xh, flags);
+  gemm_bt64<EPI_GATE_XRES><<<dim3(32, 16), blk, 0, stream>>>(yat, WoT, bob, x1, 4096, 1024, 1024, gada + 2048, xs, xh, flags);
   ln_mod<<<4096, blk, 0, stream>>>(x1, gada, msb);
   gemm_bt<EPI_GELU><<<dim3(32, 32), blk, 0, stream>>>(msb, W1T, b1b, hid, 4096, 4096, 1024, nullptr, nullptr, nullptr, nullptr);
-  gemm_bt<EPI_GATE_OUT><<<dim3(32, 8), blk, 0, stream>>>(hid, W2T, b2b, d_out, 4096, 1024, 4096, gada + 5120, x1, nullptr, flags);
-}
+  gemm_bt64<EPI_GATE_OUT><<<dim3(32, 16), blk, 0, stream>>>(hid, W2T, b2b, d_out, 4096, 1024, 4096, gada + 5120, x1, nullptr, flags);
+}
```

New measurement: 706.7 us. 1.09x faster.
